# Performance work log

Measured on AMD Instinct MI355X. Metric: run time of the kernel, lower is better.

Reference implementation:

```python
import jax, jax.numpy as jnp
import numpy as np

B, L, D = 32, 128, 128


def setup_inputs() -> dict:
    key = jax.random.key(0)
    ks = jax.random.split(key, 10)
    s = 1.0 / np.sqrt(D)  # torch nn.Linear default init bound
    inp = {
        "input_real": jax.random.normal(ks[0], (B, L, D), jnp.float32),
        "input_imag": jax.random.normal(ks[1], (B, L, D), jnp.float32),
        "Wr1": jax.random.uniform(ks[2], (D, D), jnp.float32, -s, s),
        "br1": jax.random.uniform(ks[3], (D,), jnp.float32, -s, s),
        "Wi1": jax.random.uniform(ks[4], (D, D), jnp.float32, -s, s),
        "bi1": jax.random.uniform(ks[5], (D,), jnp.float32, -s, s),
        "Wr2": jax.random.uniform(ks[6], (D, D), jnp.float32, -s, s),
        "br2": jax.random.uniform(ks[7], (D,), jnp.float32, -s, s),
        "Wi2": jax.random.uniform(ks[8], (D, D), jnp.float32, -s, s),
        "bi2": jax.random.uniform(ks[9], (D,), jnp.float32, -s, s),
    }
    return inp


def reference(input_real, input_imag, Wr1, br1, Wi1, bi1, Wr2, br2, Wi2, bi2):
    # torch Linear: y = x @ W.T + b
    r1 = input_real @ Wr1.T + br1            # (B, L, D)
    i1 = input_imag @ Wi1.T + bi1
    diag_real1 = r1 * r1 - i1 * i1           # Re((r1+i*i1)^2)
    diag_imag1 = 2.0 * r1 * i1               # Im((r1+i*i1)^2)

    r2 = input_real @ Wr2.T + br2
    i2 = input_imag @ Wi2.T + bi2
    diag_real2 = r2 * r2 - i2 * i2
    diag_imag2 = 2.0 * r2 * i2

    # attention over sequence positions L
    att_real = jax.nn.softmax(jnp.sum(diag_real1 * diag_real2, axis=-1), axis=-1)  # (B, L)
    att_imag = jax.nn.softmax(jnp.sum(diag_imag1 * diag_imag2, axis=-1), axis=-1)  # (B, L)

    # Weighted sum over L of per-token complex outer products, without
    # materializing the (B, L, D, D) intermediates the torch code builds:
    # Matrix_real[l] = r2 r2^T - i2 i2^T ; Matrix_imag[l] = i2 r2^T + r2 i2^T
    Mr = (jnp.einsum('bl,bld,ble->bde', att_real, r2, r2)
          - jnp.einsum('bl,bld,ble->bde', att_real, i2, i2))   # (B, D, D)
    Mi = (jnp.einsum('bl,bld,ble->bde', att_imag, i2, r2)
          + jnp.einsum('bl,bld,ble->bde', att_imag, r2, i2))   # (B, D, D)
    return (Mr, Mi)
```

## Files before the change

### kernel.cpp

```cpp
#include <hip/hip_runtime.h>
#include <hip/hip_bf16.h>
#include <math.h>

#define NB 32
#define NL 128
#define ND 128

typedef __attribute__((ext_vector_type(8))) short bf16x8;
typedef __attribute__((ext_vector_type(4))) float f32x4;

union F4  { float4 v; float f[4]; };
union BF8 { bf16x8 v; ushort u[8]; };

__device__ inline ushort f2bf(float f) {
    __hip_bfloat16 h = __float2bfloat16(f);
    union { __hip_bfloat16 h; ushort u; } c; c.h = h; return c.u;
}
__device__ inline float bf2f(ushort u) {
    union { unsigned int i; float f; } c; c.i = ((unsigned int)u) << 16; return c.f;
}
__device__ inline short2 bsplit(float f) {
    ushort hu = f2bf(f);
    short2 r;
    r.x = (short)hu;
    r.y = (short)f2bf(f - bf2f(hu));
    return r;
}

__global__ __launch_bounds__(256, 1) void k_one(
    const float* __restrict__ xr, const float* __restrict__ xi,
    const float* __restrict__ Wr1, const float* __restrict__ br1,
    const float* __restrict__ Wi1, const float* __restrict__ bi1,
    const float* __restrict__ Wr2, const float* __restrict__ br2,
    const float* __restrict__ Wi2, const float* __restrict__ bi2,
    float* __restrict__ out)
{
    extern __shared__ char L[];
    char*  Wb   = L + 65536;
    float* lgs  = (float*)(L + 131072);
    float* wfl  = (float*)(L + 132096);
    float* wred = (float*)(L + 132608);

    const int t     = threadIdx.x;
    const int w     = t >> 6;
    const int lane  = t & 63;
    const int l15   = lane & 15;
    const int koff8 = (lane >> 4) * 8;
    const int koffb = koff8 * 2;

    const int bid  = blockIdx.x;
    const int b    = bid >> 3;
    const int sub  = bid & 7;
    const int term = sub >> 2;
    const int dq   = (sub >> 1) & 1;
    const int eo   = sub & 1;

    const int srow = (t >> 2) & 15;
    const float* Wsrc = (w == 0) ? Wr1 : (w == 1) ? Wi1 : (w == 2) ? Wr2 : Wi2;

    F4 wpf[8];

#define LOADW(NT)                                                             \
    {                                                                         \
        const float* p = Wsrc + (size_t)((NT) * 16 + srow) * ND;              \
        _Pragma("unroll")                                                     \
        for (int j = 0; j < 8; ++j)                                           \
            wpf[j].v = *(const float4*)&p[((t & 3) + 4 * j) * 4];             \
    }

#define WRITEW(BUF)                                                           \
    {                                                                         \
        char* mb = Wb + (BUF) * 32768 + w * 8192 + srow * 256;                \
        const int sw = (srow & 7) << 4;                                       \
        _Pragma("unroll")                                                     \
        for (int j = 0; j < 8; ++j) {                                         \
            short2 s0 = bsplit(wpf[j].f[0]), s1 = bsplit(wpf[j].f[1]);        \
            short2 s2 = bsplit(wpf[j].f[2]), s3 = bsplit(wpf[j].f[3]);        \
            int kb = ((t & 3) + 4 * j) * 8;                                   \
            ushort4 hh = {(ushort)s0.x, (ushort)s1.x, (ushort)s2.x, (ushort)s3.x}; \
            ushort4 ll = {(ushort)s0.y, (ushort)s1.y, (ushort)s2.y, (ushort)s3.y}; \
            *(ushort4*)(mb + (kb ^ sw))        = hh;                          \
            *(ushort4*)(mb + 4096 + (kb ^ sw)) = ll;                          \
        }                                                                     \
    }

    bf16x8 axh[2][2][4], axl[2][2][4];
    {
        const float* xs[2] = {xr, xi};
#pragma unroll
        for (int lt2 = 0; lt2 < 2; ++lt2) {
            const int arowg = b * NL + (w + 4 * lt2) * 16 + l15;
#pragma unroll
            for (int arr = 0; arr < 2; ++arr)
#pragma unroll
                for (int ks = 0; ks < 4; ++ks) {
                    const float* p = xs[arr] + (size_t)arowg * ND + ks * 32 + koff8;
                    F4 f0, f1;
                    f0.v = *(const float4*)&p[0];
                    f1.v = *(const float4*)&p[4];
                    bf16x8 h, l;
#pragma unroll
                    for (int e = 0; e < 4; ++e) {
                        short2 s = bsplit(f0.f[e]); h[e] = s.x; l[e] = s.y;
                    }
#pragma unroll
                    for (int e = 0; e < 4; ++e) {
                        short2 s = bsplit(f1.f[e]); h[4 + e] = s.x; l[4 + e] = s.y;
                    }
                    axh[lt2][arr][ks] = h;
                    axl[lt2][arr][ks] = l;
                }
        }
    }

    float pR[2][4] = {{0.f,0.f,0.f,0.f},{0.f,0.f,0.f,0.f}};
    float pI[2][4] = {{0.f,0.f,0.f,0.f},{0.f,0.f,0.f,0.f}};

    LOADW(0)
    WRITEW(0)
    __syncthreads();

    for (int nt = 0; nt < 8; ++nt) {
        if (nt < 7) LOADW(nt + 1)

        f32x4 acc[4][2];
#pragma unroll
        for (int m = 0; m < 4; ++m)
#pragma unroll
            for (int lt2 = 0; lt2 < 2; ++lt2)
                acc[m][lt2] = (f32x4){0.f, 0.f, 0.f, 0.f};

        {
            const char* bufp = Wb + (nt & 1) * 32768 + l15 * 256;
            const int swr = (l15 & 7) << 4;
#pragma unroll
            for (int mat = 0; mat < 4; ++mat) {
                const int arr = mat & 1;
                const char* mb = bufp + mat * 8192;
#pragma unroll
                for (int ks = 0; ks < 4; ++ks) {
                    const int off = ((ks * 64) + koffb) ^ swr;
                    bf16x8 bh = *(const bf16x8*)(mb + off);
                    bf16x8 bl = *(const bf16x8*)(mb + 4096 + off);
                    acc[mat][0] = __builtin_amdgcn_mfma_f32_16x16x32_bf16(axh[0][arr][ks], bh, acc[mat][0], 0, 0, 0);
                    acc[mat][0] = __builtin_amdgcn_mfma_f32_16x16x32_bf16(axh[0][arr][ks], bl, acc[mat][0], 0, 0, 0);
                    acc[mat][0] = __builtin_amdgcn_mfma_f32_16x16x32_bf16(axl[0][arr][ks], bh, acc[mat][0], 0, 0, 0);
                    acc[mat][1] = __builtin_amdgcn_mfma_f32_16x16x32_bf16(axh[1][arr][ks], bh, acc[mat][1], 0, 0, 0);
                    acc[mat][1] = __builtin_amdgcn_mfma_f32_16x16x32_bf16(axh[1][arr][ks], bl, acc[mat][1], 0, 0, 0);
                    acc[mat][1] = __builtin_amdgcn_mfma_f32_16x16x32_bf16(axl[1][arr][ks], bh, acc[mat][1], 0, 0, 0);
                }
            }
        }

        {
            const int d  = nt * 16 + l15;
            const float b0 = br1[d], b1 = bi1[d], b2 = br2[d], b3 = bi2[d];
#pragma unroll
            for (int lt2 = 0; lt2 < 2; ++lt2) {
                const int lb = (w + 4 * lt2) * 16 + (lane >> 4) * 4;
                ushort g2[4], g3[4];
#pragma unroll
                for (int r = 0; r < 4; ++r) {
                    float y0 = acc[0][lt2][r] + b0;
                    float y1 = acc[1][lt2][r] + b1;
                    float y2 = acc[2][lt2][r] + b2;
                    float y3 = acc[3][lt2][r] + b3;
                    pR[lt2][r] += (y0 * y0 - y1 * y1) * (y2 * y2 - y3 * y3);
                    pI[lt2][r] += 4.f * y0 * y1 * y2 * y3;
                    g2[r] = f2bf(y2);
                    g3[r] = f2bf(y3);
                }
                const int byte0 = d * 256 + ((lb * 2) ^ ((d & 7) << 4));
                *(unsigned int*)(L + byte0)             = (unsigned int)g2[0] | ((unsigned int)g2[1] << 16);
                *(unsigned int*)(L + byte0 + 4)         = (unsigned int)g2[2] | ((unsigned int)g2[3] << 16);
                *(unsigned int*)(L + 32768 + byte0)     = (unsigned int)g3[0] | ((unsigned int)g3[1] << 16);
                *(unsigned int*)(L + 32768 + byte0 + 4) = (unsigned int)g3[2] | ((unsigned int)g3[3] << 16);
            }
        }

        __syncthreads();
        if (nt < 7) {
            WRITEW((nt + 1) & 1)
            __syncthreads();
        }
    }

#pragma unroll
    for (int off = 1; off < 16; off <<= 1)
#pragma unroll
        for (int lt2 = 0; lt2 < 2; ++lt2)
#pragma unroll
            for (int r = 0; r < 4; ++r) {
                pR[lt2][r] += __shfl_xor(pR[lt2][r], off);
                pI[lt2][r] += __shfl_xor(pI[lt2][r], off);
            }
    if (l15 == 0) {
#pragma unroll
        for (int lt2 = 0; lt2 < 2; ++lt2) {
            const int row = (w + 4 * lt2) * 16 + (lane >> 4) * 4;
#pragma unroll
            for (int r = 0; r < 4; ++r) {
                lgs[row + r]       = pR[lt2][r];
                lgs[128 + row + r] = pI[lt2][r];
            }
        }
    }
    __syncthreads();

    float sv = 0.f, se = 0.f;
    if (t < 128) {
        sv = lgs[term * 128 + t];
        float m = sv;
#pragma unroll
        for (int off = 1; off < 64; off <<= 1) m = fmaxf(m, __shfl_xor(m, off));
        if (lane == 0) wred[w] = m;
    }
    __syncthreads();
    if (t < 128) {
        float m = fmaxf(wred[0], wred[1]);
        se = expf(sv - m);
        float s = se;
#pragma unroll
        for (int off = 1; off < 64; off <<= 1) s += __shfl_xor(s, off);
        if (lane == 0) wred[2 + w] = s;
    }
    __syncthreads();
    if (t < 128) wfl[t] = se / (wred[2] + wred[3]);
    __syncthreads();

    f32x4 accP[4], accN[4];
#pragma unroll
    for (int nt = 0; nt < 4; ++nt) {
        accP[nt] = (f32x4){0.f, 0.f, 0.f, 0.f};
        accN[nt] = (f32x4){0.f, 0.f, 0.f, 0.f};
    }

#pragma unroll
    for (int ks = 0; ks < 4; ++ks) {
        F4 w0, w1;
        w0.v = *(const float4*)&wfl[ks * 32 + koff8];
        w1.v = *(const float4*)&wfl[ks * 32 + koff8 + 4];
        float wv[8] = {w0.f[0], w0.f[1], w0.f[2], w0.f[3],
                       w1.f[0], w1.f[1], w1.f[2], w1.f[3]};

        const int ar = dq * 64 + w * 16 + l15;
        const int ab = ar * 256 + (((ks * 64) + koffb) ^ ((ar & 7) << 4));
        BF8 a0; a0.v = *(const bf16x8*)(L + ab);
        BF8 a1; a1.v = *(const bf16x8*)(L + 32768 + ab);
        bf16x8 s0, s1;
#pragma unroll
        for (int e = 0; e < 8; ++e) {
            s0[e] = (short)f2bf(bf2f(a0.u[e]) * wv[e]);
            s1[e] = (short)f2bf(bf2f(a1.u[e]) * wv[e]);
        }
        bf16x8 aP = term ? s1 : s0;
        bf16x8 aN = term ? s0 : s1;

#pragma unroll
        for (int nt = 0; nt < 4; ++nt) {
            const int br = eo * 64 + nt * 16 + l15;
            const int bb = br * 256 + (((ks * 64) + koffb) ^ ((br & 7) << 4));
            bf16x8 b0 = *(const bf16x8*)(L + bb);
            bf16x8 b1 = *(const bf16x8*)(L + 32768 + bb);
            accP[nt] = __builtin_amdgcn_mfma_f32_16x16x32_bf16(aP, b0, accP[nt], 0, 0, 0);
            accN[nt] = __builtin_amdgcn_mfma_f32_16x16x32_bf16(aN, b1, accN[nt], 0, 0, 0);
        }
    }

    const float sgn = term ? 1.f : -1.f;
    float* dst = out + (size_t)term * NB * ND * ND + (size_t)b * ND * ND;
    const int rb = dq * 64 + w * 16 + (lane >> 4) * 4;
#pragma unroll
    for (int nt = 0; nt < 4; ++nt) {
        const int ec = eo * 64 + nt * 16 + l15;
#pragma unroll
        for (int r = 0; r < 4; ++r)
            dst[(size_t)(rb + r) * ND + ec] = accP[nt][r] + sgn * accN[nt][r];
    }
}

extern "C" void kernel_launch(void* const* d_in, const int* in_sizes, int n_in,
                              void* d_out, int out_size, void* d_ws, size_t ws_size,
                              hipStream_t stream)
{
    const float* xr  = (const float*)d_in[0];
    const float* xi  = (const float*)d_in[1];
    const float* Wr1 = (const float*)d_in[2];
    const float* br1 = (const float*)d_in[3];
    const float* Wi1 = (const float*)d_in[4];
    const float* bi1 = (const float*)d_in[5];
    const float* Wr2 = (const float*)d_in[6];
    const float* br2 = (const float*)d_in[7];
    const float* Wi2 = (const float*)d_in[8];
    const float* bi2 = (const float*)d_in[9];

    (void)hipFuncSetAttribute((const void*)k_one,
                              hipFuncAttributeMaxDynamicSharedMemorySize, 132672);

    hipLaunchKernelGGL(k_one, dim3(256), dim3(256), 132672, stream,
                       xr, xi, Wr1, br1, Wi1, bi1, Wr2, br2, Wi2, bi2,
                       (float*)d_out);
}
```

Baseline: 29.69 us.

## Double block size to 512 threads and split projection and outer-product work across 8 waves

The block goes from 256 to 512 threads. In the projection each wave now owns one 16-row L tile instead of two, and in the outer-product GEMM each wave owns two N-tiles instead of four. The staging of the next W tile into shared memory moves before the epilogue, which removes one __syncthreads per iteration. The weight load is reorganised so each thread writes 16-byte bf16x8 vectors. This doubles the waves available to hide latency and halves per-wave register state, at the cost of more threads contending for the same LDS and barriers.

```diff
diff --git a/kernel.cpp b/kernel.cpp
--- a/kernel.cpp
+++ b/kernel.cpp
@@ -27,7 +27,7 @@
     return r;
 }
 
-__global__ __launch_bounds__(256, 1) void k_one(
+__global__ __launch_bounds__(512, 1) void k_one(
     const float* __restrict__ xr, const float* __restrict__ xi,
     const float* __restrict__ Wr1, const float* __restrict__ br1,
     const float* __restrict__ Wi1, const float* __restrict__ bi1,
@@ -55,66 +55,68 @@
     const int dq   = (sub >> 1) & 1;
     const int eo   = sub & 1;
 
-    const int srow = (t >> 2) & 15;
-    const float* Wsrc = (w == 0) ? Wr1 : (w == 1) ? Wi1 : (w == 2) ? Wr2 : Wi2;
-
-    F4 wpf[8];
+    const int smat = t >> 7;
+    const int srow = (t >> 3) & 15;
+    const int skq  = t & 7;
+    const float* Wsrc = (smat == 0) ? Wr1 : (smat == 1) ? Wi1
+                      : (smat == 2) ? Wr2 : Wi2;
+
+    F4 wpf[4];
 
 #define LOADW(NT)                                                             \
     {                                                                         \
-        const float* p = Wsrc + (size_t)((NT) * 16 + srow) * ND;              \
+        const float* p = Wsrc + (size_t)((NT) * 16 + srow) * ND + skq * 16;   \
         _Pragma("unroll")                                                     \
-        for (int j = 0; j < 8; ++j)                                           \
-            wpf[j].v = *(const float4*)&p[((t & 3) + 4 * j) * 4];             \
+        for (int j = 0; j < 4; ++j)                                           \
+            wpf[j].v = *(const float4*)&p[4 * j];                             \
     }
 
 #define WRITEW(BUF)                                                           \
     {                                                                         \
-        char* mb = Wb + (BUF) * 32768 + w * 8192 + srow * 256;                \
+        char* mb = Wb + (BUF) * 32768 + smat * 8192 + srow * 256;             \
         const int sw = (srow & 7) << 4;                                       \
+        bf16x8 h0, l0, h1, l1;                                                \
         _Pragma("unroll")                                                     \
-        for (int j = 0; j < 8; ++j) {                                         \
-            short2 s0 = bsplit(wpf[j].f[0]), s1 = bsplit(wpf[j].f[1]);        \
-            short2 s2 = bsplit(wpf[j].f[2]), s3 = bsplit(wpf[j].f[3]);        \
-            int kb = ((t & 3) + 4 * j) * 8;                                   \
-            ushort4 hh = {(ushort)s0.x, (ushort)s1.x, (ushort)s2.x, (ushort)s3.x}; \
-            ushort4 ll = {(ushort)s0.y, (ushort)s1.y, (ushort)s2.y, (ushort)s3.y}; \
-            *(ushort4*)(mb + (kb ^ sw))        = hh;                          \
-            *(ushort4*)(mb + 4096 + (kb ^ sw)) = ll;                          \
+        for (int e = 0; e < 4; ++e) {                                         \
+            short2 sa = bsplit(wpf[0].f[e]); h0[e] = sa.x; l0[e] = sa.y;      \
+            short2 sb = bsplit(wpf[1].f[e]); h0[4 + e] = sb.x; l0[4 + e] = sb.y; \
+            short2 sc = bsplit(wpf[2].f[e]); h1[e] = sc.x; l1[e] = sc.y;      \
+            short2 sd = bsplit(wpf[3].f[e]); h1[4 + e] = sd.x; l1[4 + e] = sd.y; \
         }                                                                     \
-    }
-
-    bf16x8 axh[2][2][4], axl[2][2][4];
+        *(bf16x8*)(mb + ((skq * 32) ^ sw))             = h0;                  \
+        *(bf16x8*)(mb + ((skq * 32 + 16) ^ sw))        = h1;                  \
+        *(bf16x8*)(mb + 4096 + ((skq * 32) ^ sw))      = l0;                  \
+        *(bf16x8*)(mb + 4096 + ((skq * 32 + 16) ^ sw)) = l1;                  \
+    }
+
+    bf16x8 axh[2][4], axl[2][4];
     {
         const float* xs[2] = {xr, xi};
-#pragma unroll
-        for (int lt2 = 0; lt2 < 2; ++lt2) {
-            const int arowg = b * NL + (w + 4 * lt2) * 16 + l15;
-#pragma unroll
-            for (int arr = 0; arr < 2; ++arr)
-#pragma unroll
-                for (int ks = 0; ks < 4; ++ks) {
-                    const float* p = xs[arr] + (size_t)arowg * ND + ks * 32 + koff8;
-                    F4 f0, f1;
-                    f0.v = *(const float4*)&p[0];
-                    f1.v = *(const float4*)&p[4];
-                    bf16x8 h, l;
-#pragma unroll
-                    for (int e = 0; e < 4; ++e) {
-                        short2 s = bsplit(f0.f[e]); h[e] = s.x; l[e] = s.y;
-                    }
-#pragma unroll
-                    for (int e = 0; e < 4; ++e) {
-                        short2 s = bsplit(f1.f[e]); h[4 + e] = s.x; l[4 + e] = s.y;
-                    }
-                    axh[lt2][arr][ks] = h;
-                    axl[lt2][arr][ks] = l;
+        const int arowg = b * NL + w * 16 + l15;
+#pragma unroll
+        for (int arr = 0; arr < 2; ++arr)
+#pragma unroll
+            for (int ks = 0; ks < 4; ++ks) {
+                const float* p = xs[arr] + (size_t)arowg * ND + ks * 32 + koff8;
+                F4 f0, f1;
+                f0.v = *(const float4*)&p[0];
+                f1.v = *(const float4*)&p[4];
+                bf16x8 h, l;
+#pragma unroll
+                for (int e = 0; e < 4; ++e) {
+                    short2 s = bsplit(f0.f[e]); h[e] = s.x; l[e] = s.y;
                 }
-        }
-    }
-
-    float pR[2][4] = {{0.f,0.f,0.f,0.f},{0.f,0.f,0.f,0.f}};
-    float pI[2][4] = {{0.f,0.f,0.f,0.f},{0.f,0.f,0.f,0.f}};
+#pragma unroll
+                for (int e = 0; e < 4; ++e) {
+                    short2 s = bsplit(f1.f[e]); h[4 + e] = s.x; l[4 + e] = s.y;
+                }
+                axh[arr][ks] = h;
+                axl[arr][ks] = l;
+            }
+    }
+
+    float pR[4] = {0.f, 0.f, 0.f, 0.f};
+    float pI[4] = {0.f, 0.f, 0.f, 0.f};
 
     LOADW(0)
     WRITEW(0)
@@ -123,12 +125,9 @@
     for (int nt = 0; nt < 8; ++nt) {
         if (nt < 7) LOADW(nt + 1)
 
-        f32x4 acc[4][2];
-#pragma unroll
-        for (int m = 0; m < 4; ++m)
-#pragma unroll
-            for (int lt2 = 0; lt2 < 2; ++lt2)
-                acc[m][lt2] = (f32x4){0.f, 0.f, 0.f, 0.f};
+        f32x4 acc[4];
+#pragma unroll
+        for (int m = 0; m < 4; ++m) acc[m] = (f32x4){0.f, 0.f, 0.f, 0.f};
 
         {
             const char* bufp = Wb + (nt & 1) * 32768 + l15 * 256;
@@ -142,67 +141,54 @@
                     const int off = ((ks * 64) + koffb) ^ swr;
                     bf16x8 bh = *(const bf16x8*)(mb + off);
                     bf16x8 bl = *(const bf16x8*)(mb + 4096 + off);
-                    acc[mat][0] = __builtin_amdgcn_mfma_f32_16x16x32_bf16(axh[0][arr][ks], bh, acc[mat][0], 0, 0, 0);
-                    acc[mat][0] = __builtin_amdgcn_mfma_f32_16x16x32_bf16(axh[0][arr][ks], bl, acc[mat][0], 0, 0, 0);
-                    acc[mat][0] = __builtin_amdgcn_mfma_f32_16x16x32_bf16(axl[0][arr][ks], bh, acc[mat][0], 0, 0, 0);
-                    acc[mat][1] = __builtin_amdgcn_mfma_f32_16x16x32_bf16(axh[1][arr][ks], bh, acc[mat][1], 0, 0, 0);
-                    acc[mat][1] = __builtin_amdgcn_mfma_f32_16x16x32_bf16(axh[1][arr][ks], bl, acc[mat][1], 0, 0, 0);
-                    acc[mat][1] = __builtin_amdgcn_mfma_f32_16x16x32_bf16(axl[1][arr][ks], bh, acc[mat][1], 0, 0, 0);
+                    acc[mat] = __builtin_amdgcn_mfma_f32_16x16x32_bf16(axh[arr][ks], bh, acc[mat], 0, 0, 0);
+                    acc[mat] = __builtin_amdgcn_mfma_f32_16x16x32_bf16(axh[arr][ks], bl, acc[mat], 0, 0, 0);
+                    acc[mat] = __builtin_amdgcn_mfma_f32_16x16x32_bf16(axl[arr][ks], bh, acc[mat], 0, 0, 0);
                 }
             }
         }
+
+        if (nt < 7) WRITEW((nt + 1) & 1)
 
         {
             const int d  = nt * 16 + l15;
             const float b0 = br1[d], b1 = bi1[d], b2 = br2[d], b3 = bi2[d];
-#pragma unroll
-            for (int lt2 = 0; lt2 < 2; ++lt2) {
-                const int lb = (w + 4 * lt2) * 16 + (lane >> 4) * 4;
-                ushort g2[4], g3[4];
-#pragma unroll
-                for (int r = 0; r < 4; ++r) {
-                    float y0 = acc[0][lt2][r] + b0;
-                    float y1 = acc[1][lt2][r] + b1;
-                    float y2 = acc[2][lt2][r] + b2;
-                    float y3 = acc[3][lt2][r] + b3;
-                    pR[lt2][r] += (y0 * y0 - y1 * y1) * (y2 * y2 - y3 * y3);
-                    pI[lt2][r] += 4.f * y0 * y1 * y2 * y3;
-                    g2[r] = f2bf(y2);
-                    g3[r] = f2bf(y3);
-                }
-                const int byte0 = d * 256 + ((lb * 2) ^ ((d & 7) << 4));
-                *(unsigned int*)(L + byte0)             = (unsigned int)g2[0] | ((unsigned int)g2[1] << 16);
-                *(unsigned int*)(L + byte0 + 4)         = (unsigned int)g2[2] | ((unsigned int)g2[3] << 16);
-                *(unsigned int*)(L + 32768 + byte0)     = (unsigned int)g3[0] | ((unsigned int)g3[1] << 16);
-                *(unsigned int*)(L + 32768 + byte0 + 4) = (unsigned int)g3[2] | ((unsigned int)g3[3] << 16);
+            const int lb = w * 16 + (lane >> 4) * 4;
+            ushort g2[4], g3[4];
+#pragma unroll
+            for (int r = 0; r < 4; ++r) {
+                float y0 = acc[0][r] + b0;
+                float y1 = acc[1][r] + b1;
+                float y2 = acc[2][r] + b2;
+                float y3 = acc[3][r] + b3;
+                pR[r] += (y0 * y0 - y1 * y1) * (y2 * y2 - y3 * y3);
+                pI[r] += 4.f * y0 * y1 * y2 * y3;
+                g2[r] = f2bf(y2);
+                g3[r] = f2bf(y3);
             }
+            const int byte0 = d * 256 + ((lb * 2) ^ ((d & 7) << 4));
+            *(unsigned int*)(L + byte0)             = (unsigned int)g2[0] | ((unsigned int)g2[1] << 16);
+            *(unsigned int*)(L + byte0 + 4)         = (unsigned int)g2[2] | ((unsigned int)g2[3] << 16);
+            *(unsigned int*)(L + 32768 + byte0)     = (unsigned int)g3[0] | ((unsigned int)g3[1] << 16);
+            *(unsigned int*)(L + 32768 + byte0 + 4) = (unsigned int)g3[2] | ((unsigned int)g3[3] << 16);
         }
 
         __syncthreads();
-        if (nt < 7) {
-            WRITEW((nt + 1) & 1)
-            __syncthreads();
-        }
     }
 
 #pragma unroll
     for (int off = 1; off < 16; off <<= 1)
 #pragma unroll
-        for (int lt2 = 0; lt2 < 2; ++lt2)
-#pragma unroll
-            for (int r = 0; r < 4; ++r) {
-                pR[lt2][r] += __shfl_xor(pR[lt2][r], off);
-                pI[lt2][r] += __shfl_xor(pI[lt2][r], off);
-            }
+        for (int r = 0; r < 4; ++r) {
+            pR[r] += __shfl_xor(pR[r], off);
+            pI[r] += __shfl_xor(pI[r], off);
+        }
     if (l15 == 0) {
-#pragma unroll
-        for (int lt2 = 0; lt2 < 2; ++lt2) {
-            const int row = (w + 4 * lt2) * 16 + (lane >> 4) * 4;
-#pragma unroll
-            for (int r = 0; r < 4; ++r) {
-                lgs[row + r]       = pR[lt2][r];
-                lgs[128 + row + r] = pI[lt2][r];
-            }
+        const int row = w * 16 + (lane >> 4) * 4;
+#pragma unroll
+        for (int r = 0; r < 4; ++r) {
+            lgs[row + r]       = pR[r];
+            lgs[128 + row + r] = pI[r];
         }
     }
     __syncthreads();
@@ -228,11 +214,14 @@
     if (t < 128) wfl[t] = se / (wred[2] + wred[3]);
     __syncthreads();
 
-    f32x4 accP[4], accN[4];
-#pragma unroll
-    for (int nt = 0; nt < 4; ++nt) {
-        accP[nt] = (f32x4){0.f, 0.f, 0.f, 0.f};
-        accN[nt] = (f32x4){0.f, 0.f, 0.f, 0.f};
+    const int mt  = w & 3;
+    const int ntp = w >> 2;
+
+    f32x4 accP[2], accN[2];
+#pragma unroll
+    for (int n = 0; n < 2; ++n) {
+        accP[n] = (f32x4){0.f, 0.f, 0.f, 0.f};
+        accN[n] = (f32x4){0.f, 0.f, 0.f, 0.f};
     }
 
 #pragma unroll
@@ -243,7 +232,7 @@
         float wv[8] = {w0.f[0], w0.f[1], w0.f[2], w0.f[3],
                        w1.f[0], w1.f[1], w1.f[2], w1.f[3]};
 
-        const int ar = dq * 64 + w * 16 + l15;
+        const int ar = dq * 64 + mt * 16 + l15;
         const int ab = ar * 256 + (((ks * 64) + koffb) ^ ((ar & 7) << 4));
         BF8 a0; a0.v = *(const bf16x8*)(L + ab);
         BF8 a1; a1.v = *(const bf16x8*)(L + 32768 + ab);
@@ -257,25 +246,25 @@
         bf16x8 aN = term ? s0 : s1;
 
 #pragma unroll
-        for (int nt = 0; nt < 4; ++nt) {
-            const int br = eo * 64 + nt * 16 + l15;
+        for (int n = 0; n < 2; ++n) {
+            const int br = eo * 64 + (ntp * 2 + n) * 16 + l15;
             const int bb = br * 256 + (((ks * 64) + koffb) ^ ((br & 7) << 4));
             bf16x8 b0 = *(const bf16x8*)(L + bb);
             bf16x8 b1 = *(const bf16x8*)(L + 32768 + bb);
-            accP[nt] = __builtin_amdgcn_mfma_f32_16x16x32_bf16(aP, b0, accP[nt], 0, 0, 0);
-            accN[nt] = __builtin_amdgcn_mfma_f32_16x16x32_bf16(aN, b1, accN[nt], 0, 0, 0);
+            accP[n] = __builtin_amdgcn_mfma_f32_16x16x32_bf16(aP, b0, accP[n], 0, 0, 0);
+            accN[n] = __builtin_amdgcn_mfma_f32_16x16x32_bf16(aN, b1, accN[n], 0, 0, 0);
         }
     }
 
     const float sgn = term ? 1.f : -1.f;
     float* dst = out + (size_t)term * NB * ND * ND + (size_t)b * ND * ND;
-    const int rb = dq * 64 + w * 16 + (lane >> 4) * 4;
-#pragma unroll
-    for (int nt = 0; nt < 4; ++nt) {
-        const int ec = eo * 64 + nt * 16 + l15;
+    const int rb = dq * 64 + mt * 16 + (lane >> 4) * 4;
+#pragma unroll
+    for (int n = 0; n < 2; ++n) {
+        const int ec = eo * 64 + (ntp * 2 + n) * 16 + l15;
 #pragma unroll
         for (int r = 0; r < 4; ++r)
-            dst[(size_t)(rb + r) * ND + ec] = accP[nt][r] + sgn * accN[nt][r];
+            dst[(size_t)(rb + r) * ND + ec] = accP[n][r] + sgn * accN[n][r];
     }
 }
 
@@ -297,7 +286,7 @@
     (void)hipFuncSetAttribute((const void*)k_one,
                               hipFuncAttributeMaxDynamicSharedMemorySize, 132672);
 
-    hipLaunchKernelGGL(k_one, dim3(256), dim3(256), 132672, stream,
+    hipLaunchKernelGGL(k_one, dim3(256), dim3(512), 132672, stream,
                        xr, xi, Wr1, br1, Wi1, bi1, Wr2, br2, Wi2, bi2,
                        (float*)d_out);
 }
```

New measurement: 25.86 us. 1.15x faster.
